# Kernel tuning notes

Hardware: AMD Instinct MI355X
Metric: run time of the kernel (lower is better)

The kernel has to match this reference:

```python
import jax, jax.numpy as jnp
import numpy as np

ALPHA_MGD = 2e-05
NOISE_SIGMA = 8.0
NOISE_VAR = NOISE_SIGMA ** 2  # 64.0


def _conv2d(x, w, b, pad):
    # x: [N,C,H,W], w: [O,I,kh,kw]
    y = jax.lax.conv_general_dilated(
        x, w, window_strides=(1, 1), padding=[(pad, pad), (pad, pad)],
        dimension_numbers=("NCHW", "OIHW", "NCHW"))
    return y + b[None, :, None, None]


def setup_inputs() -> dict:
    key = jax.random.key(0)
    ks = jax.random.split(key, 8)
    N, Cs, Ct, H, W = 8, 128, 256, 64, 64
    return {
        "preds_S": jax.random.normal(ks[0], (N, Cs, H, W), jnp.float32),
        "preds_T": jax.random.normal(ks[1], (N, Ct, H, W), jnp.float32),
        "W_align": jax.random.normal(ks[2], (Ct, Cs, 1, 1), jnp.float32) * 0.05,
        "b_align": jnp.zeros((Ct,), jnp.float32),
        "W_gen1": jax.random.normal(ks[3], (Ct, Ct, 3, 3), jnp.float32) * 0.02,
        "b_gen1": jnp.zeros((Ct,), jnp.float32),
        "W_gen2": jax.random.normal(ks[4], (Ct, Ct, 3, 3), jnp.float32) * 0.02,
        "b_gen2": jnp.zeros((Ct,), jnp.float32),
    }


def reference(preds_S, preds_T, W_align, b_align, W_gen1, b_gen1, W_gen2, b_gen2):
    # align student channels to teacher channels (1x1 conv)
    s = _conv2d(preds_S, W_align, b_align, pad=0)
    N, C, H, W = preds_T.shape
    # deterministic checkerboard mask: tile([[0,1],[1,0]]) cropped to HxW -> (h+w) % 2
    hh = jnp.arange(H)[:, None]
    ww = jnp.arange(W)[None, :]
    mat = ((hh + ww) % 2).astype(s.dtype)  # [H,W]
    masked_fea = s * mat  # broadcast over [N,C,H,W]
    # generation network: conv3x3 -> relu -> conv3x3
    new_fea = _conv2d(jax.nn.relu(_conv2d(masked_fea, W_gen1, b_gen1, pad=1)), W_gen2, b_gen2, pad=1)
    # bmc_loss_md(pred=preds_T, target=new_fea, noise_var=64):
    # logits[i,j] = MVN(pred_i, noise_var*I).log_prob(target_j); the normalization
    # constant is class-independent and cancels in cross-entropy, keep the quadratic term.
    p = preds_T.reshape(N, -1)   # [N, D], D = C*H*W
    t = new_fea.reshape(N, -1)   # [N, D]
    # pairwise squared L2 via ||p||^2 + ||t||^2 - 2 p.t  (avoids NxNxD blow-up)
    sq = (jnp.sum(p * p, axis=1)[:, None]
          + jnp.sum(t * t, axis=1)[None, :]
          - 2.0 * (p @ t.T))  # [N, N]
    logits = -0.5 * sq / NOISE_VAR
    # cross_entropy(logits, arange(N)) = mean_i (logsumexp_j logits[i,j] - logits[i,i])
    ce = jnp.mean(jax.nn.logsumexp(logits, axis=1) - jnp.diagonal(logits))
    loss = ce * (2.0 * NOISE_VAR) / N
    return loss * ALPHA_MGD
```

## Files before the change

kernel.cpp:

```cpp
#include <hip/hip_runtime.h>

typedef unsigned short u16;
typedef short short8 __attribute__((ext_vector_type(8)));
typedef unsigned short ushort8 __attribute__((ext_vector_type(8)));
typedef float floatx16 __attribute__((ext_vector_type(16)));

#define PLANE8   34848
#define NSTRIDE  1115136

__device__ __forceinline__ u16 f2b(float f) {
  unsigned u = __builtin_bit_cast(unsigned, f);
  return (u16)((u + 0x7FFFu + ((u >> 16) & 1u)) >> 16);
}
__device__ __forceinline__ float b2f(u16 b) {
  return __builtin_bit_cast(float, ((unsigned)b) << 16);
}

typedef const __attribute__((address_space(1))) unsigned int* gptr_t;
typedef __attribute__((address_space(3))) unsigned int* sptr_t;

__global__ __launch_bounds__(256) void kprep(
    const float* __restrict__ Wg1, u16* __restrict__ Wsw1,
    const float* __restrict__ Wg2, u16* __restrict__ Wsw2,
    const float* __restrict__ Wa,  u16* __restrict__ Wb,
    const float* __restrict__ pS,  u16* __restrict__ T,
    u16* __restrict__ masked, u16* __restrict__ t1)
{
  __shared__ u16 Ls[64 * 136];
  int b = blockIdx.x, t = threadIdx.x;

  if (b < 576) {
    const float* W = (b < 288) ? Wg1 : Wg2;
    u16* D = (b < 288) ? Wsw1 : Wsw2;
    int bb = (b < 288) ? b : b - 288;
    int cid = bb * 256 + t;
    int d = cid % 1152, ctcg = cid / 1152;
    int ct = ctcg & 3, cg = ctcg >> 2;
    int colow = d & 31, cihalf = (d >> 5) & 1, sc = (d >> 6) & 1, tap = d >> 7;
    int co = ct * 64 + sc * 32 + colow;
    short8 v;
    #pragma unroll
    for (int jj = 0; jj < 8; ++jj) {
      int ci = cg * 16 + cihalf * 8 + jj;
      v[jj] = (short)f2b(W[((size_t)(co * 256 + ci)) * 9 + tap]);
    }
    *(short8*)&D[(size_t)cid * 8] = v;
  } else if (b < 592) {
    int v = (b - 576) * 256 + t;
    int colow = v & 31, hfb = (v >> 5) & 1, cog = (v >> 6) & 7, k = v >> 9;
    int co = cog * 32 + colow;
    int ci0 = k * 16 + hfb * 8;
    float4 f0 = *(const float4*)(Wa + (size_t)co * 128 + ci0);
    float4 f1 = *(const float4*)(Wa + (size_t)co * 128 + ci0 + 4);
    short8 o;
    o[0] = (short)f2b(f0.x); o[1] = (short)f2b(f0.y);
    o[2] = (short)f2b(f0.z); o[3] = (short)f2b(f0.w);
    o[4] = (short)f2b(f1.x); o[5] = (short)f2b(f1.y);
    o[6] = (short)f2b(f1.z); o[7] = (short)f2b(f1.w);
    *(short8*)&Wb[(size_t)v * 8] = o;
  } else if (b < 1104) {
    int bb = b - 592;
    int n = bb >> 6, pt = bb & 63, pix0 = pt * 64;
    int ci = t >> 1, ph = t & 1;
    const float* src = pS + ((size_t)n * 128 + ci) * 4096 + pix0 + ph * 32;
    #pragma unroll
    for (int i = 0; i < 8; ++i) {
      float4 v4 = *(const float4*)(src + i * 4);
      int pix = ph * 32 + i * 4;
      Ls[(pix + 0) * 136 + ci] = f2b(v4.x);
      Ls[(pix + 1) * 136 + ci] = f2b(v4.y);
      Ls[(pix + 2) * 136 + ci] = f2b(v4.z);
      Ls[(pix + 3) * 136 + ci] = f2b(v4.w);
    }
    __syncthreads();
    int p = t >> 2, q = t & 3;
    const u16* row = Ls + p * 136 + q * 32;
    u16* dst = T + ((size_t)n * 4096 + pix0 + p) * 128 + q * 32;
    #pragma unroll
    for (int k2 = 0; k2 < 4; ++k2)
      *(ushort8*)(dst + k2 * 8) = *(const ushort8*)(row + k2 * 8);
  } else {
    int p = b - 1104;
    u16* base = ((p >> 8) ? t1 : masked);
    int q = p & 255;
    base += (size_t)(q >> 5) * NSTRIDE + (size_t)(q & 31) * PLANE8;
    short8 z;
    #pragma unroll
    for (int jj = 0; jj < 8; ++jj) z[jj] = 0;
    #pragma unroll
    for (int pass = 0; pass < 2; ++pass) {
      int seg = t + pass * 256;
      if (seg < 264) {
        int off;
        if (seg < 66)       off = seg * 8;
        else if (seg < 132) off = (65 * 66 + (seg - 66)) * 8;
        else if (seg < 198) off = ((seg - 132) * 66) * 8;
        else                off = ((seg - 198) * 66 + 65) * 8;
        *(short8*)(base + off) = z;
      }
    }
  }
}

__global__ __launch_bounds__(256) void k1m(const u16* __restrict__ T,
    const u16* __restrict__ Wb, const float* __restrict__ ba,
    u16* __restrict__ mk)
{
  __shared__ __align__(16) u16 Wl[32768];
  int b = blockIdx.x;
  int n = b >> 5, pt = b & 31;
  int t = threadIdx.x, wid = t >> 6, lane = t & 63;
  int ml = lane & 31, hf = lane >> 5;

  #pragma unroll
  for (int kk = 0; kk < 16; ++kk) {
    int chunk = kk * 256 + t;
    __builtin_amdgcn_global_load_lds((gptr_t)(const void*)(Wb + (size_t)chunk * 8),
                                     (sptr_t)(void*)(Wl + chunk * 8), 16, 0, 0);
  }

  const u16* Tn = T + (size_t)n * 524288;
  const u16* ap[4];
  #pragma unroll
  for (int g = 0; g < 4; ++g)
    ap[g] = Tn + (size_t)(pt * 128 + g * 32 + ml) * 128 + hf * 8;

  floatx16 acc[2][4];
  #pragma unroll
  for (int q = 0; q < 2; ++q)
    #pragma unroll
    for (int g = 0; g < 4; ++g)
      #pragma unroll
      for (int i = 0; i < 16; ++i) acc[q][g][i] = 0.f;

  __syncthreads();

  const short8* WlV = (const short8*)Wl;
  int cogb = wid * 2;

  short8 a0[4], a1[4];
  #pragma unroll
  for (int g = 0; g < 4; ++g) a0[g] = *(const short8*)(ap[g]);

#define K1M_STEP(K, CUR, NXT, LAST)                                           \
  {                                                                           \
    if (!(LAST)) {                                                            \
      _Pragma("unroll")                                                       \
      for (int g = 0; g < 4; ++g)                                             \
        NXT[g] = *(const short8*)(ap[g] + ((K) + 1) * 16);                    \
    }                                                                         \
    short8 w0 = WlV[((K) * 8 + cogb) * 64 + lane];                            \
    short8 w1 = WlV[((K) * 8 + cogb + 1) * 64 + lane];                        \
    _Pragma("unroll")                                                         \
    for (int g = 0; g < 4; ++g) {                                             \
      acc[0][g] = __builtin_amdgcn_mfma_f32_32x32x16_bf16(CUR[g], w0, acc[0][g], 0, 0, 0); \
      acc[1][g] = __builtin_amdgcn_mfma_f32_32x32x16_bf16(CUR[g], w1, acc[1][g], 0, 0, 0); \
    }                                                                         \
  }
  K1M_STEP(0, a0, a1, 0)
  K1M_STEP(1, a1, a0, 0)
  K1M_STEP(2, a0, a1, 0)
  K1M_STEP(3, a1, a0, 0)
  K1M_STEP(4, a0, a1, 0)
  K1M_STEP(5, a1, a0, 0)
  K1M_STEP(6, a0, a1, 0)
  K1M_STEP(7, a1, a0, 1)
#undef K1M_STEP

  int co0 = cogb * 32 + ml, co1 = co0 + 32;
  float b0 = ba[co0], b1 = ba[co1];
  u16* base0 = mk + (size_t)n * NSTRIDE + (size_t)(co0 >> 3) * PLANE8 + (co0 & 7);
  u16* base1 = mk + (size_t)n * NSTRIDE + (size_t)(co1 >> 3) * PLANE8 + (co1 & 7);
  #pragma unroll
  for (int g = 0; g < 4; ++g)
    #pragma unroll
    for (int reg = 0; reg < 16; ++reg) {
      int m = (reg & 3) + 8 * (reg >> 2) + 4 * hf;
      int pix = pt * 128 + g * 32 + m;
      int h = pix >> 6, w = pix & 63;
      float msk = (float)((h + w) & 1);
      int off = ((h + 1) * 66 + (w + 1)) * 8;
      base0[off] = f2b((acc[0][g][reg] + b0) * msk);
      base1[off] = f2b((acc[1][g][reg] + b1) * msk);
    }
}

template <int MODE>
__global__ __launch_bounds__(128) void kconv(
    const u16* __restrict__ IN, const u16* __restrict__ WS,
    const float* __restrict__ bg, u16* __restrict__ OUT)
{
  __shared__ __align__(16) u16 LinA[896 * 8];
  __shared__ __align__(16) u16 LinB[896 * 8];
  __shared__ __align__(16) u16 LwA[1152 * 8];
  __shared__ __align__(16) u16 LwB[1152 * 8];

  int b = blockIdx.x;
  int rt = b & 15, ct = (b >> 4) & 3, n = b >> 6;
  int h0 = rt * 4;
  int t = threadIdx.x;
  int wid = t >> 6, lane = t & 63;
  int hf = lane >> 5, ml = lane & 31;

  int in_goff[7];
  int lds_off[7];
  #pragma unroll
  for (int k = 0; k < 7; ++k) {
    int seg = 2 * k + wid;
    int half = seg >= 7 ? 1 : 0;
    int s = seg - half * 7;
    in_goff[k] = half * PLANE8 + (h0 * 66 + s * 64 + lane) * 8;
    lds_off[k] = (half * 448 + s * 64) * 8;
  }

  const u16* inb = IN + (size_t)n * NSTRIDE;
  const u16* wg  = WS + (size_t)ct * 1152 * 8;

  floatx16 acc[2][2][2];
  #pragma unroll
  for (int r = 0; r < 2; ++r)
    #pragma unroll
    for (int s = 0; s < 2; ++s)
      #pragma unroll
      for (int q = 0; q < 2; ++q)
        #pragma unroll
        for (int i = 0; i < 16; ++i) acc[r][s][q][i] = 0.f;

  auto STAGE = [&](int cg, u16* LinD, u16* LwD) {
    #pragma unroll
    for (int k = 0; k < 9; ++k) {
      int sidx = wid + 2 * k;
      const u16* src = wg + (size_t)cg * 36864 + (size_t)(sidx * 64 + lane) * 8;
      __builtin_amdgcn_global_load_lds((gptr_t)(const void*)src,
                                       (sptr_t)(void*)(LwD + sidx * 512), 16, 0, 0);
    }
    #pragma unroll
    for (int k = 0; k < 7; ++k) {
      const u16* src = inb + (size_t)cg * 69696 + in_goff[k];
      __builtin_amdgcn_global_load_lds((gptr_t)(const void*)src,
                                       (sptr_t)(void*)(LinD + lds_off[k]), 16, 0, 0);
    }
  };

  auto COMPUTE = [&](const u16* LinS, const u16* LwS) {
    const short8* LinV = (const short8*)LinS;
    const short8* LwV  = (const short8*)LwS;
    #pragma unroll
    for (int dr = 0; dr < 3; ++dr) {
      int r0 = hf * 448 + (2 * wid + dr) * 66;
      int r1 = r0 + 66;
      #pragma unroll
      for (int dc = 0; dc < 3; ++dc) {
        int tap = dr * 3 + dc;
        short8 w0 = LwV[tap * 128 + lane];
        short8 w1 = LwV[tap * 128 + 64 + lane];
        short8 i00 = LinV[r0 + ml + dc];
        short8 i01 = LinV[r0 + 32 + ml + dc];
        short8 i10 = LinV[r1 + ml + dc];
        short8 i11 = LinV[r1 + 32 + ml + dc];
        acc[0][0][0] = __builtin_amdgcn_mfma_f32_32x32x16_bf16(i00, w0, acc[0][0][0], 0, 0, 0);
        acc[0][0][1] = __builtin_amdgcn_mfma_f32_32x32x16_bf16(i00, w1, acc[0][0][1], 0, 0, 0);
        acc[0][1][0] = __builtin_amdgcn_mfma_f32_32x32x16_bf16(i01, w0, acc[0][1][0], 0, 0, 0);
        acc[0][1][1] = __builtin_amdgcn_mfma_f32_32x32x16_bf16(i01, w1, acc[0][1][1], 0, 0, 0);
        acc[1][0][0] = __builtin_amdgcn_mfma_f32_32x32x16_bf16(i10, w0, acc[1][0][0], 0, 0, 0);
        acc[1][0][1] = __builtin_amdgcn_mfma_f32_32x32x16_bf16(i10, w1, acc[1][0][1], 0, 0, 0);
        acc[1][1][0] = __builtin_amdgcn_mfma_f32_32x32x16_bf16(i11, w0, acc[1][1][0], 0, 0, 0);
        acc[1][1][1] = __builtin_amdgcn_mfma_f32_32x32x16_bf16(i11, w1, acc[1][1][1], 0, 0, 0);
      }
    }
  };

  STAGE(0, LinA, LwA);
  __syncthreads();
  for (int cg = 0; cg < 16; cg += 2) {
    STAGE(cg + 1, LinB, LwB);
    COMPUTE(LinA, LwA);
    __syncthreads();
    if (cg + 2 < 16) STAGE(cg + 2, LinA, LwA);
    COMPUTE(LinB, LwB);
    __syncthreads();
  }

  float bias0 = bg[ct * 64 + ml];
  float bias1 = bg[ct * 64 + 32 + ml];

  if (MODE == 0) {
    u16* ob = OUT + (size_t)n * NSTRIDE;
    int co0 = ct * 64 + ml, co1 = co0 + 32;
    int cb0 = ((co0 >> 4) * 2 + ((co0 >> 3) & 1)) * PLANE8 + (co0 & 7);
    int cb1 = ((co1 >> 4) * 2 + ((co1 >> 3) & 1)) * PLANE8 + (co1 & 7);
    #pragma unroll
    for (int r = 0; r < 2; ++r) {
      int rowoff = (h0 + 2 * wid + r + 1) * 66 + 1;
      #pragma unroll
      for (int reg = 0; reg < 16; ++reg) {
        int m = (reg & 3) + 8 * (reg >> 2) + 4 * hf;
        float v;
        v = acc[r][0][0][reg] + bias0; v = fmaxf(v, 0.f); ob[cb0 + (rowoff + m) * 8] = f2b(v);
        v = acc[r][0][1][reg] + bias1; v = fmaxf(v, 0.f); ob[cb1 + (rowoff + m) * 8] = f2b(v);
        v = acc[r][1][0][reg] + bias0; v = fmaxf(v, 0.f); ob[cb0 + (rowoff + 32 + m) * 8] = f2b(v);
        v = acc[r][1][1][reg] + bias1; v = fmaxf(v, 0.f); ob[cb1 + (rowoff + 32 + m) * 8] = f2b(v);
      }
    }
  } else {
    u16* plane = (wid == 0) ? LinA : LwA;
    #pragma unroll
    for (int r = 0; r < 2; ++r) {
      __syncthreads();
      #pragma unroll
      for (int reg = 0; reg < 16; ++reg) {
        int m = (reg & 3) + 8 * (reg >> 2) + 4 * hf;
        plane[ml * 68 + m]              = f2b(acc[r][0][0][reg] + bias0);
        plane[(32 + ml) * 68 + m]       = f2b(acc[r][0][1][reg] + bias1);
        plane[ml * 68 + 32 + m]         = f2b(acc[r][1][0][reg] + bias0);
        plane[(32 + ml) * 68 + 32 + m]  = f2b(acc[r][1][1][reg] + bias1);
      }
      __syncthreads();
      const u16* row = plane + lane * 68;
      __align__(16) u16 tmp[64];
      #pragma unroll
      for (int k2 = 0; k2 < 16; ++k2)
        *(ushort4*)(tmp + k2 * 4) = *(const ushort4*)(row + k2 * 4);
      u16* gdst = OUT + (size_t)n * 1048576 + (size_t)(ct * 64 + lane) * 4096
                  + (h0 + 2 * wid + r) * 64;
      #pragma unroll
      for (int k2 = 0; k2 < 8; ++k2)
        *(ushort8*)(gdst + k2 * 8) = *(const ushort8*)(tmp + k2 * 8);
    }
  }
}

__global__ __launch_bounds__(256) void kbmc(const u16* __restrict__ t2,
    const float* __restrict__ pT, float* __restrict__ part)
{
  int t = threadIdx.x, lane = t & 63, role = t >> 6;
  int ih = role >> 1, nh = role & 1;
  int bid = blockIdx.x;

  float pt[4][4], pp[4], tt[4];
  #pragma unroll
  for (int i = 0; i < 4; ++i) {
    pp[i] = 0.f; tt[i] = 0.f;
    #pragma unroll
    for (int j = 0; j < 4; ++j) pt[i][j] = 0.f;
  }

  const float* pb = pT + ((size_t)ih * 4) * 1048576;
  const u16*   tb = t2 + ((size_t)nh * 4) * 1048576;

  for (int k = 0; k < 8; ++k) {
    size_t d0 = ((size_t)(bid * 512 + k * 64 + lane)) * 4;
    float4 p[4], tf[4];
    #pragma unroll
    for (int i = 0; i < 4; ++i)
      p[i] = *(const float4*)(pb + (size_t)i * 1048576 + d0);
    #pragma unroll
    for (int j = 0; j < 4; ++j) {
      ushort4 tv = *(const ushort4*)(tb + (size_t)j * 1048576 + d0);
      tf[j] = make_float4(b2f(tv.x), b2f(tv.y), b2f(tv.z), b2f(tv.w));
    }
    if (nh == 0) {
      #pragma unroll
      for (int i = 0; i < 4; ++i)
        pp[i] += p[i].x * p[i].x + p[i].y * p[i].y + p[i].z * p[i].z + p[i].w * p[i].w;
    }
    if (ih == 0) {
      #pragma unroll
      for (int j = 0; j < 4; ++j)
        tt[j] += tf[j].x * tf[j].x + tf[j].y * tf[j].y + tf[j].z * tf[j].z + tf[j].w * tf[j].w;
    }
    #pragma unroll
    for (int i = 0; i < 4; ++i)
      #pragma unroll
      for (int j = 0; j < 4; ++j)
        pt[i][j] += p[i].x * tf[j].x + p[i].y * tf[j].y
                  + p[i].z * tf[j].z + p[i].w * tf[j].w;
  }

  #pragma unroll
  for (int m = 1; m < 64; m <<= 1) {
    #pragma unroll
    for (int i = 0; i < 4; ++i) {
      pp[i] += __shfl_xor(pp[i], m);
      tt[i] += __shfl_xor(tt[i], m);
      #pragma unroll
      for (int j = 0; j < 4; ++j) pt[i][j] += __shfl_xor(pt[i][j], m);
    }
  }
  if (lane == 0) {
    #pragma unroll
    for (int i = 0; i < 4; ++i)
      #pragma unroll
      for (int j = 0; j < 4; ++j)
        part[(size_t)(16 + (ih * 4 + i) * 8 + (nh * 4 + j)) * 512 + bid] = pt[i][j];
    if (nh == 0) {
      #pragma unroll
      for (int i = 0; i < 4; ++i) part[(size_t)(ih * 4 + i) * 512 + bid] = pp[i];
    }
    if (ih == 0) {
      #pragma unroll
      for (int j = 0; j < 4; ++j) part[(size_t)(8 + nh * 4 + j) * 512 + bid] = tt[j];
    }
  }
}

__global__ __launch_bounds__(256) void kred(const float* __restrict__ part,
                                            float* __restrict__ accums)
{
  __shared__ float r4[4];
  int s = blockIdx.x, t = threadIdx.x, lane = t & 63, wid = t >> 6;
  float v = part[(size_t)s * 512 + t] + part[(size_t)s * 512 + 256 + t];
  #pragma unroll
  for (int m = 1; m < 64; m <<= 1) v += __shfl_xor(v, m);
  if (lane == 0) r4[wid] = v;
  __syncthreads();
  if (t == 0) accums[s] = r4[0] + r4[1] + r4[2] + r4[3];
}

__global__ void k4_final(const float* __restrict__ accums, float* __restrict__ out)
{
  int t = threadIdx.x;
  int i = t >> 3, j = t & 7;
  double pp = accums[i];
  double tt = accums[8 + j];
  double pt = accums[16 + i * 8 + j];
  double logit = -0.5 * (pp + tt - 2.0 * pt) / 64.0;
  double m = logit;
  #pragma unroll
  for (int s = 1; s < 8; s <<= 1) {
    double o = __shfl_xor(m, s);
    m = o > m ? o : m;
  }
  double e = exp(logit - m);
  #pragma unroll
  for (int s = 1; s < 8; s <<= 1) e += __shfl_xor(e, s);
  double lse = m + log(e);
  double term = (j == i) ? (lse - logit) : 0.0;
  #pragma unroll
  for (int s = 1; s < 64; s <<= 1) term += __shfl_xor(term, s);
  if (t == 0) {
    double ce = term / 8.0;
    out[0] = (float)(ce * (2.0 * 64.0) / 8.0 * 2e-05);
  }
}

extern "C" void kernel_launch(void* const* d_in, const int* in_sizes, int n_in,
                              void* d_out, int out_size, void* d_ws, size_t ws_size,
                              hipStream_t stream)
{
  const float* preds_S = (const float*)d_in[0];
  const float* preds_T = (const float*)d_in[1];
  const float* W_align = (const float*)d_in[2];
  const float* b_align = (const float*)d_in[3];
  const float* W_gen1  = (const float*)d_in[4];
  const float* b_gen1  = (const float*)d_in[5];
  const float* W_gen2  = (const float*)d_in[6];
  const float* b_gen2  = (const float*)d_in[7];
  float* out = (float*)d_out;

  char* wsb = (char*)d_ws;
  u16* masked = (u16*)wsb;
  u16* t1     = (u16*)(wsb + 17842176);
  u16* t2p    = (u16*)(wsb + 35684352);
  u16* T      = t2p;
  u16* Wsw1   = (u16*)(wsb + 52461568);
  u16* Wsw2   = (u16*)(wsb + 53641216);
  float* part   = (float*)(wsb + 54820864);
  float* accums = (float*)(wsb + 55017472);
  u16* Wb     = (u16*)(wsb + 55017856);

  kprep<<<1616, 256, 0, stream>>>(W_gen1, Wsw1, W_gen2, Wsw2, W_align, Wb,
                                  preds_S, T, masked, t1);
  k1m<<<256, 256, 0, stream>>>(T, Wb, b_align, masked);
  kconv<0><<<512, 128, 0, stream>>>(masked, Wsw1, b_gen1, t1);
  kconv<1><<<512, 128, 0, stream>>>(t1, Wsw2, b_gen2, t2p);
  kbmc<<<512, 256, 0, stream>>>(t2p, preds_T, part);
  kred<<<80, 256, 0, stream>>>(part, accums);
  k4_final<<<1, 64, 0, stream>>>(accums, out);
}
```

Before: 210.9 us.

## Split conv work across four waves per block and fuse final reductions

```diff
diff --git a/kernel.cpp b/kernel.cpp
--- a/kernel.cpp
+++ b/kernel.cpp
@@ -186,7 +186,7 @@
 }
 
 template <int MODE>
-__global__ __launch_bounds__(128) void kconv(
+__global__ __launch_bounds__(256) void kconv(
     const u16* __restrict__ IN, const u16* __restrict__ WS,
     const float* __restrict__ bg, u16* __restrict__ OUT)
 {
@@ -202,43 +202,39 @@
   int wid = t >> 6, lane = t & 63;
   int hf = lane >> 5, ml = lane & 31;
 
-  int in_goff[7];
-  int lds_off[7];
-  #pragma unroll
-  for (int k = 0; k < 7; ++k) {
-    int seg = 2 * k + wid;
-    int half = seg >= 7 ? 1 : 0;
-    int s = seg - half * 7;
-    in_goff[k] = half * PLANE8 + (h0 * 66 + s * 64 + lane) * 8;
-    lds_off[k] = (half * 448 + s * 64) * 8;
-  }
-
   const u16* inb = IN + (size_t)n * NSTRIDE;
   const u16* wg  = WS + (size_t)ct * 1152 * 8;
 
-  floatx16 acc[2][2][2];
-  #pragma unroll
-  for (int r = 0; r < 2; ++r)
-    #pragma unroll
-    for (int s = 0; s < 2; ++s)
-      #pragma unroll
-      for (int q = 0; q < 2; ++q)
-        #pragma unroll
-        for (int i = 0; i < 16; ++i) acc[r][s][q][i] = 0.f;
+  floatx16 acc[2][2];
+  #pragma unroll
+  for (int s = 0; s < 2; ++s)
+    #pragma unroll
+    for (int q = 0; q < 2; ++q)
+      #pragma unroll
+      for (int i = 0; i < 16; ++i) acc[s][q][i] = 0.f;
 
   auto STAGE = [&](int cg, u16* LinD, u16* LwD) {
     #pragma unroll
-    for (int k = 0; k < 9; ++k) {
-      int sidx = wid + 2 * k;
-      const u16* src = wg + (size_t)cg * 36864 + (size_t)(sidx * 64 + lane) * 8;
-      __builtin_amdgcn_global_load_lds((gptr_t)(const void*)src,
-                                       (sptr_t)(void*)(LwD + sidx * 512), 16, 0, 0);
-    }
-    #pragma unroll
-    for (int k = 0; k < 7; ++k) {
-      const u16* src = inb + (size_t)cg * 69696 + in_goff[k];
-      __builtin_amdgcn_global_load_lds((gptr_t)(const void*)src,
-                                       (sptr_t)(void*)(LinD + lds_off[k]), 16, 0, 0);
+    for (int k = 0; k < 5; ++k) {
+      int sidx = 4 * k + wid;
+      if (sidx < 18) {
+        const u16* src = wg + (size_t)cg * 36864 + (size_t)(sidx * 64 + lane) * 8;
+        __builtin_amdgcn_global_load_lds((gptr_t)(const void*)src,
+                                         (sptr_t)(void*)(LwD + sidx * 512), 16, 0, 0);
+      }
+    }
+    #pragma unroll
+    for (int k = 0; k < 4; ++k) {
+      int seg = 4 * k + wid;
+      if (seg < 14) {
+        int half = seg >= 7 ? 1 : 0;
+        int s = seg - half * 7;
+        const u16* src = inb + (size_t)cg * 69696 + half * PLANE8
+                         + (size_t)(h0 * 66 + s * 64 + lane) * 8;
+        __builtin_amdgcn_global_load_lds((gptr_t)(const void*)src,
+                                         (sptr_t)(void*)(LinD + (half * 448 + s * 64) * 8),
+                                         16, 0, 0);
+      }
     }
   };
 
@@ -247,25 +243,18 @@
     const short8* LwV  = (const short8*)LwS;
     #pragma unroll
     for (int dr = 0; dr < 3; ++dr) {
-      int r0 = hf * 448 + (2 * wid + dr) * 66;
-      int r1 = r0 + 66;
+      int r0 = hf * 448 + (wid + dr) * 66;
       #pragma unroll
       for (int dc = 0; dc < 3; ++dc) {
         int tap = dr * 3 + dc;
         short8 w0 = LwV[tap * 128 + lane];
         short8 w1 = LwV[tap * 128 + 64 + lane];
-        short8 i00 = LinV[r0 + ml + dc];
-        short8 i01 = LinV[r0 + 32 + ml + dc];
-        short8 i10 = LinV[r1 + ml + dc];
-        short8 i11 = LinV[r1 + 32 + ml + dc];
-        acc[0][0][0] = __builtin_amdgcn_mfma_f32_32x32x16_bf16(i00, w0, acc[0][0][0], 0, 0, 0);
-        acc[0][0][1] = __builtin_amdgcn_mfma_f32_32x32x16_bf16(i00, w1, acc[0][0][1], 0, 0, 0);
-        acc[0][1][0] = __builtin_amdgcn_mfma_f32_32x32x16_bf16(i01, w0, acc[0][1][0], 0, 0, 0);
-        acc[0][1][1] = __builtin_amdgcn_mfma_f32_32x32x16_bf16(i01, w1, acc[0][1][1], 0, 0, 0);
-        acc[1][0][0] = __builtin_amdgcn_mfma_f32_32x32x16_bf16(i10, w0, acc[1][0][0], 0, 0, 0);
-        acc[1][0][1] = __builtin_amdgcn_mfma_f32_32x32x16_bf16(i10, w1, acc[1][0][1], 0, 0, 0);
-        acc[1][1][0] = __builtin_amdgcn_mfma_f32_32x32x16_bf16(i11, w0, acc[1][1][0], 0, 0, 0);
-        acc[1][1][1] = __builtin_amdgcn_mfma_f32_32x32x16_bf16(i11, w1, acc[1][1][1], 0, 0, 0);
+        short8 i0 = LinV[r0 + ml + dc];
+        short8 i1 = LinV[r0 + 32 + ml + dc];
+        acc[0][0] = __builtin_amdgcn_mfma_f32_32x32x16_bf16(i0, w0, acc[0][0], 0, 0, 0);
+        acc[0][1] = __builtin_amdgcn_mfma_f32_32x32x16_bf16(i0, w1, acc[0][1], 0, 0, 0);
+        acc[1][0] = __builtin_amdgcn_mfma_f32_32x32x16_bf16(i1, w0, acc[1][0], 0, 0, 0);
+        acc[1][1] = __builtin_amdgcn_mfma_f32_32x32x16_bf16(i1, w1, acc[1][1], 0, 0, 0);
       }
     }
   };
@@ -289,44 +278,40 @@
     int co0 = ct * 64 + ml, co1 = co0 + 32;
     int cb0 = ((co0 >> 4) * 2 + ((co0 >> 3) & 1)) * PLANE8 + (co0 & 7);
     int cb1 = ((co1 >> 4) * 2 + ((co1 >> 3) & 1)) * PLANE8 + (co1 & 7);
-    #pragma unroll
-    for (int r = 0; r < 2; ++r) {
-      int rowoff = (h0 + 2 * wid + r + 1) * 66 + 1;
-      #pragma unroll
-      for (int reg = 0; reg < 16; ++reg) {
-        int m = (reg & 3) + 8 * (reg >> 2) + 4 * hf;
-        float v;
-        v = acc[r][0][0][reg] + bias0; v = fmaxf(v, 0.f); ob[cb0 + (rowoff + m) * 8] = f2b(v);
-        v = acc[r][0][1][reg] + bias1; v = fmaxf(v, 0.f); ob[cb1 + (rowoff + m) * 8] = f2b(v);
-        v = acc[r][1][0][reg] + bias0; v = fmaxf(v, 0.f); ob[cb0 + (rowoff + 32 + m) * 8] = f2b(v);
-        v = acc[r][1][1][reg] + bias1; v = fmaxf(v, 0.f); ob[cb1 + (rowoff + 32 + m) * 8] = f2b(v);
-      }
+    int rowoff = (h0 + wid + 1) * 66 + 1;
+    #pragma unroll
+    for (int reg = 0; reg < 16; ++reg) {
+      int m = (reg & 3) + 8 * (reg >> 2) + 4 * hf;
+      float v;
+      v = acc[0][0][reg] + bias0; v = fmaxf(v, 0.f); ob[cb0 + (rowoff + m) * 8] = f2b(v);
+      v = acc[0][1][reg] + bias1; v = fmaxf(v, 0.f); ob[cb1 + (rowoff + m) * 8] = f2b(v);
+      v = acc[1][0][reg] + bias0; v = fmaxf(v, 0.f); ob[cb0 + (rowoff + 32 + m) * 8] = f2b(v);
+      v = acc[1][1][reg] + bias1; v = fmaxf(v, 0.f); ob[cb1 + (rowoff + 32 + m) * 8] = f2b(v);
     }
   } else {
-    u16* plane = (wid == 0) ? LinA : LwA;
-    #pragma unroll
-    for (int r = 0; r < 2; ++r) {
-      __syncthreads();
-      #pragma unroll
-      for (int reg = 0; reg < 16; ++reg) {
-        int m = (reg & 3) + 8 * (reg >> 2) + 4 * hf;
-        plane[ml * 68 + m]              = f2b(acc[r][0][0][reg] + bias0);
-        plane[(32 + ml) * 68 + m]       = f2b(acc[r][0][1][reg] + bias1);
-        plane[ml * 68 + 32 + m]         = f2b(acc[r][1][0][reg] + bias0);
-        plane[(32 + ml) * 68 + 32 + m]  = f2b(acc[r][1][1][reg] + bias1);
-      }
-      __syncthreads();
-      const u16* row = plane + lane * 68;
-      __align__(16) u16 tmp[64];
-      #pragma unroll
-      for (int k2 = 0; k2 < 16; ++k2)
-        *(ushort4*)(tmp + k2 * 4) = *(const ushort4*)(row + k2 * 4);
-      u16* gdst = OUT + (size_t)n * 1048576 + (size_t)(ct * 64 + lane) * 4096
-                  + (h0 + 2 * wid + r) * 64;
-      #pragma unroll
-      for (int k2 = 0; k2 < 8; ++k2)
-        *(ushort8*)(gdst + k2 * 8) = *(const ushort8*)(tmp + k2 * 8);
-    }
+    u16* plane;
+    if (wid == 0)      plane = LinA;
+    else if (wid == 1) plane = LinB;
+    else if (wid == 2) plane = LwA;
+    else               plane = LwA + 4352;
+    #pragma unroll
+    for (int reg = 0; reg < 16; ++reg) {
+      int m = (reg & 3) + 8 * (reg >> 2) + 4 * hf;
+      plane[ml * 68 + m]              = f2b(acc[0][0][reg] + bias0);
+      plane[(32 + ml) * 68 + m]       = f2b(acc[0][1][reg] + bias1);
+      plane[ml * 68 + 32 + m]         = f2b(acc[1][0][reg] + bias0);
+      plane[(32 + ml) * 68 + 32 + m]  = f2b(acc[1][1][reg] + bias1);
+    }
+    const u16* row = plane + lane * 68;
+    __align__(16) u16 tmp[64];
+    #pragma unroll
+    for (int k2 = 0; k2 < 16; ++k2)
+      *(ushort4*)(tmp + k2 * 4) = *(const ushort4*)(row + k2 * 4);
+    u16* gdst = OUT + (size_t)n * 1048576 + (size_t)(ct * 64 + lane) * 4096
+                + (h0 + wid) * 64;
+    #pragma unroll
+    for (int k2 = 0; k2 < 8; ++k2)
+      *(ushort8*)(gdst + k2 * 8) = *(const ushort8*)(tmp + k2 * 8);
   }
 }
 
@@ -404,43 +389,43 @@
   }
 }
 
-__global__ __launch_bounds__(256) void kred(const float* __restrict__ part,
-                                            float* __restrict__ accums)
-{
-  __shared__ float r4[4];
-  int s = blockIdx.x, t = threadIdx.x, lane = t & 63, wid = t >> 6;
-  float v = part[(size_t)s * 512 + t] + part[(size_t)s * 512 + 256 + t];
-  #pragma unroll
-  for (int m = 1; m < 64; m <<= 1) v += __shfl_xor(v, m);
-  if (lane == 0) r4[wid] = v;
+__global__ __launch_bounds__(256) void k4f(const float* __restrict__ part,
+                                           float* __restrict__ out)
+{
+  __shared__ float acs[96];
+  int t = threadIdx.x, lane = t & 63, w = t >> 6;
+  for (int s = w; s < 96; s += 4) {
+    float v = 0.f;
+    #pragma unroll
+    for (int k = 0; k < 8; ++k) v += part[(size_t)s * 512 + k * 64 + lane];
+    #pragma unroll
+    for (int m = 1; m < 64; m <<= 1) v += __shfl_xor(v, m);
+    if (lane == 0) acs[s] = v;
+  }
   __syncthreads();
-  if (t == 0) accums[s] = r4[0] + r4[1] + r4[2] + r4[3];
-}
-
-__global__ void k4_final(const float* __restrict__ accums, float* __restrict__ out)
-{
-  int t = threadIdx.x;
-  int i = t >> 3, j = t & 7;
-  double pp = accums[i];
-  double tt = accums[8 + j];
-  double pt = accums[16 + i * 8 + j];
-  double logit = -0.5 * (pp + tt - 2.0 * pt) / 64.0;
-  double m = logit;
-  #pragma unroll
-  for (int s = 1; s < 8; s <<= 1) {
-    double o = __shfl_xor(m, s);
-    m = o > m ? o : m;
-  }
-  double e = exp(logit - m);
-  #pragma unroll
-  for (int s = 1; s < 8; s <<= 1) e += __shfl_xor(e, s);
-  double lse = m + log(e);
-  double term = (j == i) ? (lse - logit) : 0.0;
-  #pragma unroll
-  for (int s = 1; s < 64; s <<= 1) term += __shfl_xor(term, s);
-  if (t == 0) {
-    double ce = term / 8.0;
-    out[0] = (float)(ce * (2.0 * 64.0) / 8.0 * 2e-05);
+  if (t < 64) {
+    int i = t >> 3, j = t & 7;
+    double pp = acs[i];
+    double tt = acs[8 + j];
+    double pt = acs[16 + i * 8 + j];
+    double logit = -0.5 * (pp + tt - 2.0 * pt) / 64.0;
+    double m = logit;
+    #pragma unroll
+    for (int s = 1; s < 8; s <<= 1) {
+      double o = __shfl_xor(m, s);
+      m = o > m ? o : m;
+    }
+    double e = exp(logit - m);
+    #pragma unroll
+    for (int s = 1; s < 8; s <<= 1) e += __shfl_xor(e, s);
+    double lse = m + log(e);
+    double term = (j == i) ? (lse - logit) : 0.0;
+    #pragma unroll
+    for (int s = 1; s < 64; s <<= 1) term += __shfl_xor(term, s);
+    if (t == 0) {
+      double ce = term / 8.0;
+      out[0] = (float)(ce * (2.0 * 64.0) / 8.0 * 2e-05);
+    }
   }
 }
 
@@ -467,14 +452,14 @@
   u16* Wsw2   = (u16*)(wsb + 53641216);
   float* part   = (float*)(wsb + 54820864);
   float* accums = (float*)(wsb + 55017472);
+  (void)accums;
   u16* Wb     = (u16*)(wsb + 55017856);
 
   kprep<<<1616, 256, 0, stream>>>(W_gen1, Wsw1, W_gen2, Wsw2, W_align, Wb,
                                   preds_S, T, masked, t1);
   k1m<<<256, 256, 0, stream>>>(T, Wb, b_align, masked);
-  kconv<0><<<512, 128, 0, stream>>>(masked, Wsw1, b_gen1, t1);
-  kconv<1><<<512, 128, 0, stream>>>(t1, Wsw2, b_gen2, t2p);
+  kconv<0><<<512, 256, 0, stream>>>(masked, Wsw1, b_gen1, t1);
+  kconv<1><<<512, 256, 0, stream>>>(t1, Wsw2, b_gen2, t2p);
   kbmc<<<512, 256, 0, stream>>>(t2p, preds_T, part);
-  kred<<<80, 256, 0, stream>>>(part, accums);
-  k4_final<<<1, 64, 0, stream>>>(accums, out);
-}
+  k4f<<<1, 256, 0, stream>>>(part, out);
+}
```

Result: slower. 223.6 us (+6.0%).
